# Kernel optimization log

Hardware: AMD Instinct MI355X
Metric: run time of the kernel (lower is better)

The kernel has to match this reference:

```python
import jax, jax.numpy as jnp
import numpy as np

N = 100      # num sensors/nodes
C = 32       # channels (hard-coded in module)
H = 512      # hidden_size (hard-coded)
T = 64       # window_size (lags)
B = 16       # batch
E = 2000     # edges = N * topk
HORIZON = 10


def _arma(x, ei, ew, W, V, b, n):
    # ARMAConv, num_stacks=1, num_layers=1, GELU act, dropout off (eval)
    h = x @ W                                    # (n, C)
    row, col = ei[0], ei[1]
    deg = jax.ops.segment_sum(ew, col, num_segments=n)
    dinv = jnp.where(deg > 0, 1.0 / jnp.sqrt(jnp.maximum(deg, 1e-12)), 0.0)
    norm = dinv[row] * ew * dinv[col]            # gcn_norm, no self loops
    agg = jax.ops.segment_sum(norm[:, None] * h[row], col, num_segments=n)
    return jax.nn.gelu(agg + x @ V + b, approximate=False)


def _lstm_step(h, c, xt, Wih, Whh, bih, bhh):
    g = xt @ Wih.T + h @ Whh.T + bih + bhh
    i, f, gg, o = jnp.split(g, 4, axis=-1)       # torch gate order i,f,g,o
    c = jax.nn.sigmoid(f) * c + jax.nn.sigmoid(i) * jnp.tanh(gg)
    h = jax.nn.sigmoid(o) * jnp.tanh(c)
    return h, c


def _lstm_layer(xs, Wih, Whh, bih, bhh):
    # xs: (T, B, in) -> outputs (T, B, H), final h
    Bn = xs.shape[1]
    init = (jnp.zeros((Bn, H), xs.dtype), jnp.zeros((Bn, H), xs.dtype))
    def step(carry, xt):
        hc = _lstm_step(carry[0], carry[1], xt, Wih, Whh, bih, bhh)
        return hc, hc[0]
    (hT, cT), hs = jax.lax.scan(step, init, xs)
    return hs, hT


def setup_inputs() -> dict:
    key = jax.random.key(0)
    ks = jax.random.split(key, 20)
    s = 0.05
    def nrm(k, shape):
        return jax.random.normal(k, shape, jnp.float32) * s
    ei = jax.random.randint(ks[1], (2, E), 0, N)
    ei = ei.at[0, 0].set(N - 1).at[1, 0].set(N - 1)  # ensure max node id present
    z = lambda *sh: jnp.zeros(sh, jnp.float32)
    return {
        "window": jax.random.normal(ks[0], (B * N, T), jnp.float32),
        "edge_index": ei,
        "edge_attr": jax.random.uniform(ks[2], (E,), jnp.float32),
        "W_embed": nrm(ks[3], (N, C)),
        "tg_w": nrm(ks[4], (1, C)), "tg_v": nrm(ks[5], (1, C)), "tg_b": z(C),
        "gnn_w": nrm(ks[6], (1, C)), "gnn_v": nrm(ks[7], (1, C)), "gnn_b": z(C),
        "lstm_Wih0": nrm(ks[8], (4 * H, N * C)), "lstm_Whh0": nrm(ks[9], (4 * H, H)),
        "lstm_bih0": z(4 * H), "lstm_bhh0": z(4 * H),
        "lstm_Wih1": nrm(ks[10], (4 * H, H)), "lstm_Whh1": nrm(ks[11], (4 * H, H)),
        "lstm_bih1": z(4 * H), "lstm_bhh1": z(4 * H),
        "c1_Wih": nrm(ks[12], (4 * H, N * C)), "c1_Whh": nrm(ks[13], (4 * H, H)),
        "c1_bih": z(4 * H), "c1_bhh": z(4 * H),
        "c2_Wih": nrm(ks[14], (4 * H, H)), "c2_Whh": nrm(ks[15], (4 * H, H)),
        "c2_bih": z(4 * H), "c2_bhh": z(4 * H),
        "Wp": nrm(ks[16], (N, H)), "bp": z(N),
    }


def _forward(edge_index, window, edge_attr, W_embed, tg_w, tg_v, tg_b,
             gnn_w, gnn_v, gnn_b,
             lstm_Wih0, lstm_Whh0, lstm_bih0, lstm_bhh0,
             lstm_Wih1, lstm_Whh1, lstm_bih1, lstm_bhh1,
             c1_Wih, c1_Whh, c1_bih, c1_bhh,
             c2_Wih, c2_Whh, c2_bih, c2_bhh, Wp, bp):
    BN = B * N
    # batch edges over B (offset b*N), exactly as the torch offset arithmetic
    bi = (edge_index[:, None, :] + (jnp.arange(B) * N)[None, :, None]).reshape(2, B * E)
    battr = jnp.tile(edge_attr, B)
    # temporal batching inside TGConv: offsets t*(B*N) on node-major flat x
    ti = (bi[:, None, :] + (jnp.arange(T) * BN)[None, :, None]).reshape(2, T * B * E)
    tattr = jnp.tile(battr, T)
    x = _arma(window.reshape(BN * T, 1), ti, tattr, tg_w, tg_v, tg_b, BN * T)  # (BN*T, C)
    x = x.reshape(B, N, T, C).transpose(0, 2, 1, 3) + W_embed                 # (B,T,N,C)
    x = x.reshape(B, T, N * C).transpose(1, 0, 2)                             # (T,B,NC)
    hs0, h1f = _lstm_layer(x, lstm_Wih0, lstm_Whh0, lstm_bih0, lstm_bhh0)
    hs1, h2f = _lstm_layer(hs0, lstm_Wih1, lstm_Whh1, lstm_bih1, lstm_bhh1)
    # original assigns (h_n, h_n): cell states seeded from hidden states
    def step(carry, _):
        h1, c1, h2, c2 = carry
        pred = h2 @ Wp.T + bp                      # (B, N)
        g = _arma(pred.reshape(BN, 1), bi, battr, gnn_w, gnn_v, gnn_b, BN)
        xin = (g.reshape(B, N, C) + W_embed).reshape(B, N * C)
        h1n, c1n = _lstm_step(h1, c1, xin, c1_Wih, c1_Whh, c1_bih, c1_bhh)
        h2n, c2n = _lstm_step(h2, c2, h1n, c2_Wih, c2_Whh, c2_bih, c2_bhh)
        return (h1n, c1n, h2n, c2n), pred.reshape(-1)
    _, preds = jax.lax.scan(step, (h1f, h1f, h2f, h2f), None, length=HORIZON)
    return preds.T                                  # (B*N, HORIZON)


def reference(window, edge_index, edge_attr, W_embed, tg_w, tg_v, tg_b,
              gnn_w, gnn_v, gnn_b,
              lstm_Wih0, lstm_Whh0, lstm_bih0, lstm_bhh0,
              lstm_Wih1, lstm_Whh1, lstm_bih1, lstm_bhh1,
              c1_Wih, c1_Whh, c1_bih, c1_bhh,
              c2_Wih, c2_Whh, c2_bih, c2_bhh, Wp, bp):
    return _forward(edge_index, window, edge_attr, W_embed, tg_w, tg_v, tg_b,
                    gnn_w, gnn_v, gnn_b,
                    lstm_Wih0, lstm_Whh0, lstm_bih0, lstm_bhh0,
                    lstm_Wih1, lstm_Whh1, lstm_bih1, lstm_bhh1,
                    c1_Wih, c1_Whh, c1_bih, c1_bhh,
                    c2_Wih, c2_Whh, c2_bih, c2_bhh, Wp, bp)
```

## Files before the change

### kernel.cpp

```cpp
#include <hip/hip_runtime.h>
#include <math.h>

#define TT 64
#define HZN 10
#define NBLK 256

__device__ __forceinline__ float sigm(float x) { return 1.f / (1.f + expf(-x)); }
__device__ __forceinline__ float gelu_f(float x) { return 0.5f * x * (1.f + erff(x * 0.70710678118654752f)); }

__device__ __forceinline__ float cLd(const float* p) {
  return __hip_atomic_load(p, __ATOMIC_RELAXED, __HIP_MEMORY_SCOPE_AGENT);
}
__device__ __forceinline__ void cSt(float* p, float v) {
  __hip_atomic_store(p, v, __ATOMIC_RELAXED, __HIP_MEMORY_SCOPE_AGENT);
}

__device__ __forceinline__ void gbar(unsigned* flags, unsigned* gen,
                                     int bid, int tid, unsigned& bgen) {
  ++bgen;
  __syncthreads();
  if (bid == 0) {
    if (tid > 0 && tid < NBLK) {
      while (__hip_atomic_load(&flags[tid], __ATOMIC_RELAXED, __HIP_MEMORY_SCOPE_AGENT) < bgen)
        __builtin_amdgcn_s_sleep(1);
    }
    __syncthreads();
    if (tid == 0)
      __hip_atomic_store(gen, bgen, __ATOMIC_RELAXED, __HIP_MEMORY_SCOPE_AGENT);
  } else {
    if (tid == 0) {
      asm volatile("s_waitcnt vmcnt(0)" ::: "memory");
      __hip_atomic_store(&flags[bid], bgen, __ATOMIC_RELAXED, __HIP_MEMORY_SCOPE_AGENT);
      while (__hip_atomic_load(gen, __ATOMIC_RELAXED, __HIP_MEMORY_SCOPE_AGENT) < bgen)
        __builtin_amdgcn_s_sleep(1);
    }
    __syncthreads();
  }
}

__device__ __forceinline__ void red32(float (&a)[4][4]) {
#pragma unroll
  for (int q = 0; q < 4; ++q)
#pragma unroll
    for (int r = 0; r < 4; ++r) {
      float v = a[q][r];
      v += __shfl_xor(v, 16); v += __shfl_xor(v, 8); v += __shfl_xor(v, 4);
      v += __shfl_xor(v, 2);  v += __shfl_xor(v, 1);
      a[q][r] = v;
    }
}

__device__ __forceinline__ void red64(float (&a)[4][4]) {
#pragma unroll
  for (int q = 0; q < 4; ++q)
#pragma unroll
    for (int r = 0; r < 4; ++r) {
      float v = a[q][r];
      v += __shfl_xor(v, 32); v += __shfl_xor(v, 16); v += __shfl_xor(v, 8);
      v += __shfl_xor(v, 4);  v += __shfl_xor(v, 2);  v += __shfl_xor(v, 1);
      a[q][r] = v;
    }
}

__global__ void setup_kernel(const int* __restrict__ ei, const float* __restrict__ ew,
                             int* __restrict__ cptr, int* __restrict__ csrc, float* __restrict__ cnorm) {
  __shared__ float deg[100];
  __shared__ float dinv[100];
  __shared__ int cnt[100];
  __shared__ int pos[100];
  __shared__ int ptr[101];
  const int t = threadIdx.x;
  if (t < 100) { deg[t] = 0.f; cnt[t] = 0; }
  __syncthreads();
  for (int e = t; e < 2000; e += 256) {
    int c = ei[2000 + e];
    atomicAdd(&deg[c], ew[e]);
    atomicAdd(&cnt[c], 1);
  }
  __syncthreads();
  if (t < 100) dinv[t] = (deg[t] > 0.f) ? 1.f / sqrtf(fmaxf(deg[t], 1e-12f)) : 0.f;
  if (t == 0) {
    ptr[0] = 0;
    for (int n = 0; n < 100; ++n) ptr[n + 1] = ptr[n] + cnt[n];
  }
  __syncthreads();
  if (t < 100) pos[t] = ptr[t];
  if (t < 101) cptr[t] = ptr[t];
  __syncthreads();
  for (int e = t; e < 2000; e += 256) {
    int r = ei[e], c = ei[2000 + e];
    int p = atomicAdd(&pos[c], 1);
    csrc[p] = r;
    cnorm[p] = dinv[r] * ew[e] * dinv[c];
  }
}

__global__ void xs_kernel(const float* __restrict__ win,
                          const int* __restrict__ cptr, const int* __restrict__ csrc,
                          const float* __restrict__ cnorm,
                          const float* __restrict__ tgw, const float* __restrict__ tgv,
                          const float* __restrict__ tgb, const float* __restrict__ Wemb,
                          float* __restrict__ XS) {
  const int g = blockIdx.x * 256 + threadIdx.x;
  if (g >= 102400) return;
  const int n2 = g % 100;
  const int base = g - n2;
  float s = 0.f;
  const int p0 = cptr[n2], p1 = cptr[n2 + 1];
  for (int p = p0; p < p1; ++p) s += cnorm[p] * win[base + csrc[p]];
  const float x = win[g];
  const int t = g % 64;
  const int bb = g / 6400;
  const int n = (g / 64) % 100;
  float* dst = XS + (size_t)(t * 16 + bb) * 3200 + n * 32;
  for (int c = 0; c < 32; ++c) {
    float v = s * tgw[c] + x * tgv[c] + tgb[c];
    dst[c] = gelu_f(v) + Wemb[n * 32 + c];
  }
}

__global__ __launch_bounds__(256) void g0_gemm(const float* __restrict__ XS, const float* __restrict__ W,
                                               const float* __restrict__ b1, const float* __restrict__ b2,
                                               float* __restrict__ G0) {
  __shared__ float As[16][68];
  __shared__ float Bs[16][68];
  const int tid = threadIdx.x;
  const int m0 = blockIdx.y * 64, n0 = blockIdx.x * 64;
  const int tx = tid & 15, ty = tid >> 4;
  const int lr = tid >> 2, lk = (tid & 3) * 4;
  float acc[4][4] = {};
  for (int k0 = 0; k0 < 3200; k0 += 16) {
    float4 av = *(const float4*)&XS[(size_t)(m0 + lr) * 3200 + k0 + lk];
    float4 bv = *(const float4*)&W[(size_t)(n0 + lr) * 3200 + k0 + lk];
    As[lk + 0][lr] = av.x; As[lk + 1][lr] = av.y; As[lk + 2][lr] = av.z; As[lk + 3][lr] = av.w;
    Bs[lk + 0][lr] = bv.x; Bs[lk + 1][lr] = bv.y; Bs[lk + 2][lr] = bv.z; Bs[lk + 3][lr] = bv.w;
    __syncthreads();
#pragma unroll
    for (int kk = 0; kk < 16; ++kk) {
      float4 a = *(const float4*)&As[kk][ty * 4];
      float4 b = *(const float4*)&Bs[kk][tx * 4];
      acc[0][0] += a.x * b.x; acc[0][1] += a.x * b.y; acc[0][2] += a.x * b.z; acc[0][3] += a.x * b.w;
      acc[1][0] += a.y * b.x; acc[1][1] += a.y * b.y; acc[1][2] += a.y * b.z; acc[1][3] += a.y * b.w;
      acc[2][0] += a.z * b.x; acc[2][1] += a.z * b.y; acc[2][2] += a.z * b.z; acc[2][3] += a.z * b.w;
      acc[3][0] += a.w * b.x; acc[3][1] += a.w * b.y; acc[3][2] += a.w * b.z; acc[3][3] += a.w * b.w;
    }
    __syncthreads();
  }
#pragma unroll
  for (int i = 0; i < 4; ++i) {
    const int m = m0 + ty * 4 + i;
#pragma unroll
    for (int j = 0; j < 4; ++j) {
      const int nn = n0 + tx * 4 + j;
      G0[(size_t)m * 2048 + nn] = acc[i][j] + b1[nn] + b2[nn];
    }
  }
}

struct CoopArgs {
  const float* G0;
  const float* Whh0;
  const float* Wih1; const float* Whh1; const float* bih1; const float* bhh1;
  const float* c1Wih; const float* c1Whh; const float* c1bih; const float* c1bhh;
  const float* c2Wih; const float* c2Whh; const float* c2bih; const float* c2bhh;
  const float* Wp; const float* bp;
  const float* gw; const float* gv; const float* gb;
  const float* Wemb;
  const int* cptr; const int* csrc; const float* cnorm;
  float* hs0; float* hL1; float* c0; float* cL1;
  float* h1d; float* c1b; float* h2d; float* c2b;
  float* pred; float* xin;
  unsigned* flags; unsigned* gen;
  float* out;
};

__global__ __launch_bounds__(512, 2) void coop_kernel(CoopArgs A) {
  __shared__ float lds[16384];
  const int tid = threadIdx.x;
  const int bid = blockIdx.x;
  const int gid = bid * 512 + tid;
  unsigned bgen = 0;

  const int layer = bid >> 7;
  const int ublk = bid & 127;
  const int u0 = ublk * 4;
  const int bg = tid >> 7;
  const int du = (tid >> 5) & 3;
  const int s = tid & 31;
  const int n_s = u0 + du;

  for (int t2 = 0; t2 <= TT; ++t2) {
    if (layer == 0) {
      if (t2 < TT) {
        const int t0 = t2;
        float acc[4][4] = {};
        if (t0 > 0) {
          const float* src = A.hs0 + (size_t)(t0 - 1) * 8192;
          for (int i = tid; i < 8192; i += 512) lds[i] = cLd(&src[i]);
        }
        __syncthreads();
        if (t0 > 0) {
          for (int jj = 0; jj < 16; ++jj) {
            const int j = jj * 32 + s;
            const float w0 = A.Whh0[(n_s) * 512 + j];
            const float w1 = A.Whh0[(512 + n_s) * 512 + j];
            const float w2 = A.Whh0[(1024 + n_s) * 512 + j];
            const float w3 = A.Whh0[(1536 + n_s) * 512 + j];
#pragma unroll
            for (int br = 0; br < 4; ++br) {
              const float hv = lds[(bg * 4 + br) * 512 + j];
              acc[0][br] += w0 * hv; acc[1][br] += w1 * hv;
              acc[2][br] += w2 * hv; acc[3][br] += w3 * hv;
            }
          }
        }
        red32(acc);
        if (s == 0) {
#pragma unroll
          for (int br = 0; br < 4; ++br) {
            const int b = bg * 4 + br;
            const float* g0r = A.G0 + (size_t)(t0 * 16 + b) * 2048;
            const float gi = acc[0][br] + g0r[n_s];
            const float gf = acc[1][br] + g0r[512 + n_s];
            const float gg = acc[2][br] + g0r[1024 + n_s];
            const float go = acc[3][br] + g0r[1536 + n_s];
            const float cp = (t0 > 0) ? A.c0[b * 512 + n_s] : 0.f;
            const float cn = sigm(gf) * cp + sigm(gi) * tanhf(gg);
            const float hn = sigm(go) * tanhf(cn);
            A.c0[b * 512 + n_s] = cn;
            cSt(&A.hs0[(size_t)t0 * 8192 + b * 512 + n_s], hn);
          }
        }
      }
    } else {
      if (t2 >= 1) {
        const int t1 = t2 - 1;
        float acc[4][4] = {};
        {
          const float* sA = A.hs0 + (size_t)t1 * 8192;
          for (int i = tid; i < 8192; i += 512) lds[i] = cLd(&sA[i]);
          if (t1 > 0) {
            const float* sB = A.hL1 + (t1 & 1) * 8192;
            for (int i = tid; i < 8192; i += 512) lds[8192 + i] = cLd(&sB[i]);
          }
        }
        __syncthreads();
        for (int jj = 0; jj < 16; ++jj) {
          const int j = jj * 32 + s;
          const float wa0 = A.Wih1[(n_s) * 512 + j];
          const float wa1 = A.Wih1[(512 + n_s) * 512 + j];
          const float wa2 = A.Wih1[(1024 + n_s) * 512 + j];
          const float wa3 = A.Wih1[(1536 + n_s) * 512 + j];
#pragma unroll
          for (int br = 0; br < 4; ++br) {
            const float ha = lds[(bg * 4 + br) * 512 + j];
            acc[0][br] += wa0 * ha; acc[1][br] += wa1 * ha;
            acc[2][br] += wa2 * ha; acc[3][br] += wa3 * ha;
          }
          if (t1 > 0) {
            const float wb0 = A.Whh1[(n_s) * 512 + j];
            const float wb1 = A.Whh1[(512 + n_s) * 512 + j];
            const float wb2 = A.Whh1[(1024 + n_s) * 512 + j];
            const float wb3 = A.Whh1[(1536 + n_s) * 512 + j];
#pragma unroll
            for (int br = 0; br < 4; ++br) {
              const float hb = lds[8192 + (bg * 4 + br) * 512 + j];
              acc[0][br] += wb0 * hb; acc[1][br] += wb1 * hb;
              acc[2][br] += wb2 * hb; acc[3][br] += wb3 * hb;
            }
          }
        }
        red32(acc);
        if (s == 0) {
#pragma unroll
          for (int br = 0; br < 4; ++br) {
            const int b = bg * 4 + br;
            const float gi = acc[0][br] + A.bih1[n_s] + A.bhh1[n_s];
            const float gf = acc[1][br] + A.bih1[512 + n_s] + A.bhh1[512 + n_s];
            const float gg = acc[2][br] + A.bih1[1024 + n_s] + A.bhh1[1024 + n_s];
            const float go = acc[3][br] + A.bih1[1536 + n_s] + A.bhh1[1536 + n_s];
            const float cp = (t1 > 0) ? A.cL1[b * 512 + n_s] : 0.f;
            const float cn = sigm(gf) * cp + sigm(gi) * tanhf(gg);
            const float hn = sigm(go) * tanhf(cn);
            A.cL1[b * 512 + n_s] = cn;
            cSt(&A.hL1[((t1 & 1) ^ 1) * 8192 + b * 512 + n_s], hn);
          }
        }
      }
    }
    gbar(A.flags, A.gen, bid, tid, bgen);
  }

  if (gid < 8192) {
    const float h1v = cLd(&A.hs0[(size_t)63 * 8192 + gid]);
    cSt(&A.h1d[gid], h1v); cSt(&A.c1b[gid], h1v);
    const float h2v = cLd(&A.hL1[gid]);
    cSt(&A.h2d[gid], h2v); cSt(&A.c2b[gid], h2v);
  }
  gbar(A.flags, A.gen, bid, tid, bgen);

  for (int hz = 0; hz < HZN; ++hz) {
    const int cur = hz & 1, nxt = cur ^ 1;

    if (gid < 25600) {
      const int bn = gid >> 4, sp = gid & 15;
      const int b = bn / 100, n = bn % 100;
      const float* h2 = A.h2d + cur * 8192 + b * 512;
      const float* wp = A.Wp + n * 512;
      float a = 0.f;
      for (int jj = 0; jj < 32; ++jj) { const int j = jj * 16 + sp; a += cLd(&h2[j]) * wp[j]; }
      a += __shfl_xor(a, 1); a += __shfl_xor(a, 2); a += __shfl_xor(a, 4); a += __shfl_xor(a, 8);
      if (sp == 0) {
        const float v = a + A.bp[n];
        cSt(&A.pred[bn], v);
        A.out[bn * HZN + hz] = v;
      }
    }
    gbar(A.flags, A.gen, bid, tid, bgen);

    if (bid < 100) {
      for (int i = tid; i < 1600; i += 512) lds[i] = cLd(&A.pred[i]);
      __syncthreads();
      const int g2 = bid * 512 + tid;
      const int b = g2 / 3200, rem = g2 % 3200;
      const int n = rem >> 5, c = rem & 31;
      float s2 = 0.f;
      const int p0 = A.cptr[n], p1 = A.cptr[n + 1];
      for (int p = p0; p < p1; ++p) s2 += A.cnorm[p] * lds[b * 100 + A.csrc[p]];
      const float pv = lds[b * 100 + n];
      const float v = s2 * A.gw[c] + pv * A.gv[c] + A.gb[c];
      cSt(&A.xin[g2], gelu_f(v) + A.Wemb[n * 32 + c]);
    }
    gbar(A.flags, A.gen, bid, tid, bgen);

    {
      const int uc = bid & 63, bq = bid >> 6;
      const int u = tid >> 6, sl = tid & 63;
      const int n = uc * 8 + u;
      float* xinl = lds;
      float* h1l = lds + 12800;
      for (int i = tid; i < 12800; i += 512) xinl[i] = cLd(&A.xin[(size_t)bq * 12800 + i]);
      for (int i = tid; i < 2048; i += 512) h1l[i] = cLd(&A.h1d[cur * 8192 + bq * 2048 + i]);
      __syncthreads();
      float acc[4][4] = {};
      for (int jj = 0; jj < 50; ++jj) {
        const int j = jj * 64 + sl;
        const float w0 = A.c1Wih[(size_t)(n) * 3200 + j];
        const float w1 = A.c1Wih[(size_t)(512 + n) * 3200 + j];
        const float w2 = A.c1Wih[(size_t)(1024 + n) * 3200 + j];
        const float w3 = A.c1Wih[(size_t)(1536 + n) * 3200 + j];
#pragma unroll
        for (int bl = 0; bl < 4; ++bl) {
          const float xv = xinl[bl * 3200 + j];
          acc[0][bl] += w0 * xv; acc[1][bl] += w1 * xv;
          acc[2][bl] += w2 * xv; acc[3][bl] += w3 * xv;
        }
      }
      for (int jj = 0; jj < 8; ++jj) {
        const int j = jj * 64 + sl;
        const float w0 = A.c1Whh[(n) * 512 + j];
        const float w1 = A.c1Whh[(512 + n) * 512 + j];
        const float w2 = A.c1Whh[(1024 + n) * 512 + j];
        const float w3 = A.c1Whh[(1536 + n) * 512 + j];
#pragma unroll
        for (int bl = 0; bl < 4; ++bl) {
          const float hv = h1l[bl * 512 + j];
          acc[0][bl] += w0 * hv; acc[1][bl] += w1 * hv;
          acc[2][bl] += w2 * hv; acc[3][bl] += w3 * hv;
        }
      }
      red64(acc);
      if (sl == 0) {
#pragma unroll
        for (int bl = 0; bl < 4; ++bl) {
          const int b = bq * 4 + bl;
          const float gi = acc[0][bl] + A.c1bih[n] + A.c1bhh[n];
          const float gf = acc[1][bl] + A.c1bih[512 + n] + A.c1bhh[512 + n];
          const float gg = acc[2][bl] + A.c1bih[1024 + n] + A.c1bhh[1024 + n];
          const float go = acc[3][bl] + A.c1bih[1536 + n] + A.c1bhh[1536 + n];
          const float cp = cLd(&A.c1b[b * 512 + n]);
          const float cn = sigm(gf) * cp + sigm(gi) * tanhf(gg);
          const float hn = sigm(go) * tanhf(cn);
          cSt(&A.c1b[b * 512 + n], cn);
          cSt(&A.h1d[nxt * 8192 + b * 512 + n], hn);
        }
      }
    }
    gbar(A.flags, A.gen, bid, tid, bgen);

    {
      const int uc = bid & 63, bq = bid >> 6;
      const int u = tid >> 6, sl = tid & 63;
      const int n = uc * 8 + u;
      float* hAl = lds;
      float* hBl = lds + 2048;
      for (int i = tid; i < 2048; i += 512) {
        hAl[i] = cLd(&A.h1d[nxt * 8192 + bq * 2048 + i]);
        hBl[i] = cLd(&A.h2d[cur * 8192 + bq * 2048 + i]);
      }
      __syncthreads();
      float acc[4][4] = {};
      for (int jj = 0; jj < 8; ++jj) {
        const int j = jj * 64 + sl;
        const float wa0 = A.c2Wih[(n) * 512 + j];
        const float wa1 = A.c2Wih[(512 + n) * 512 + j];
        const float wa2 = A.c2Wih[(1024 + n) * 512 + j];
        const float wa3 = A.c2Wih[(1536 + n) * 512 + j];
        const float wb0 = A.c2Whh[(n) * 512 + j];
        const float wb1 = A.c2Whh[(512 + n) * 512 + j];
        const float wb2 = A.c2Whh[(1024 + n) * 512 + j];
        const float wb3 = A.c2Whh[(1536 + n) * 512 + j];
#pragma unroll
        for (int bl = 0; bl < 4; ++bl) {
          const float ha = hAl[bl * 512 + j];
          const float hb = hBl[bl * 512 + j];
          acc[0][bl] += wa0 * ha + wb0 * hb;
          acc[1][bl] += wa1 * ha + wb1 * hb;
          acc[2][bl] += wa2 * ha + wb2 * hb;
          acc[3][bl] += wa3 * ha + wb3 * hb;
        }
      }
      red64(acc);
      if (sl == 0) {
#pragma unroll
        for (int bl = 0; bl < 4; ++bl) {
          const int b = bq * 4 + bl;
          const float gi = acc[0][bl] + A.c2bih[n] + A.c2bhh[n];
          const float gf = acc[1][bl] + A.c2bih[512 + n] + A.c2bhh[512 + n];
          const float gg = acc[2][bl] + A.c2bih[1024 + n] + A.c2bhh[1024 + n];
          const float go = acc[3][bl] + A.c2bih[1536 + n] + A.c2bhh[1536 + n];
          const float cp = cLd(&A.c2b[b * 512 + n]);
          const float cn = sigm(gf) * cp + sigm(gi) * tanhf(gg);
          const float hn = sigm(go) * tanhf(cn);
          cSt(&A.c2b[b * 512 + n], cn);
          cSt(&A.h2d[nxt * 8192 + b * 512 + n], hn);
        }
      }
    }
    gbar(A.flags, A.gen, bid, tid, bgen);
  }
}

extern "C" void kernel_launch(void* const* d_in, const int* in_sizes, int n_in,
                              void* d_out, int out_size, void* d_ws, size_t ws_size,
                              hipStream_t stream) {
  (void)in_sizes; (void)n_in; (void)out_size; (void)ws_size;
  const float* window = (const float*)d_in[0];
  const int* ei = (const int*)d_in[1];
  const float* ew = (const float*)d_in[2];
  const float* Wemb = (const float*)d_in[3];
  const float* tgw = (const float*)d_in[4];
  const float* tgv = (const float*)d_in[5];
  const float* tgb = (const float*)d_in[6];
  const float* gw = (const float*)d_in[7];
  const float* gv = (const float*)d_in[8];
  const float* gb = (const float*)d_in[9];
  const float* Wih0 = (const float*)d_in[10];
  const float* Whh0 = (const float*)d_in[11];
  const float* bih0 = (const float*)d_in[12];
  const float* bhh0 = (const float*)d_in[13];
  const float* Wih1 = (const float*)d_in[14];
  const float* Whh1 = (const float*)d_in[15];
  const float* bih1 = (const float*)d_in[16];
  const float* bhh1 = (const float*)d_in[17];
  const float* c1Wih = (const float*)d_in[18];
  const float* c1Whh = (const float*)d_in[19];
  const float* c1bih = (const float*)d_in[20];
  const float* c1bhh = (const float*)d_in[21];
  const float* c2Wih = (const float*)d_in[22];
  const float* c2Whh = (const float*)d_in[23];
  const float* c2bih = (const float*)d_in[24];
  const float* c2bhh = (const float*)d_in[25];
  const float* Wp = (const float*)d_in[26];
  const float* bp = (const float*)d_in[27];

  char* w = (char*)d_ws;
  size_t off = 0;
  auto alloc = [&](size_t bytes) { void* p = w + off; off = (off + bytes + 255) & ~(size_t)255; return p; };
  int* cptr = (int*)alloc(101 * 4);
  int* csrc = (int*)alloc(2000 * 4);
  float* cnorm = (float*)alloc(2000 * 4);
  float* XS = (float*)alloc((size_t)1024 * 3200 * 4);
  float* G0 = (float*)alloc((size_t)1024 * 2048 * 4);
  float* hs0 = (float*)alloc((size_t)64 * 8192 * 4);
  float* hL1 = (float*)alloc((size_t)2 * 8192 * 4);
  float* c0 = (float*)alloc((size_t)8192 * 4);
  float* cL1 = (float*)alloc((size_t)8192 * 4);
  float* h1d = (float*)alloc((size_t)2 * 8192 * 4);
  float* c1b = (float*)alloc((size_t)8192 * 4);
  float* h2d = (float*)alloc((size_t)2 * 8192 * 4);
  float* c2b = (float*)alloc((size_t)8192 * 4);
  float* pred = (float*)alloc(1600 * 4);
  float* xin = (float*)alloc((size_t)51200 * 4);
  unsigned* flags = (unsigned*)alloc(NBLK * 4);
  unsigned* gen = (unsigned*)alloc(64);

  hipMemsetAsync(flags, 0, NBLK * 4, stream);
  hipMemsetAsync(gen, 0, 4, stream);

  setup_kernel<<<1, 256, 0, stream>>>(ei, ew, cptr, csrc, cnorm);
  xs_kernel<<<400, 256, 0, stream>>>(window, cptr, csrc, cnorm, tgw, tgv, tgb, Wemb, XS);
  g0_gemm<<<dim3(32, 16), 256, 0, stream>>>(XS, Wih0, bih0, bhh0, G0);

  CoopArgs A;
  A.G0 = G0; A.Whh0 = Whh0;
  A.Wih1 = Wih1; A.Whh1 = Whh1; A.bih1 = bih1; A.bhh1 = bhh1;
  A.c1Wih = c1Wih; A.c1Whh = c1Whh; A.c1bih = c1bih; A.c1bhh = c1bhh;
  A.c2Wih = c2Wih; A.c2Whh = c2Whh; A.c2bih = c2bih; A.c2bhh = c2bhh;
  A.Wp = Wp; A.bp = bp; A.gw = gw; A.gv = gv; A.gb = gb; A.Wemb = Wemb;
  A.cptr = cptr; A.csrc = csrc; A.cnorm = cnorm;
  A.hs0 = hs0; A.hL1 = hL1; A.c0 = c0; A.cL1 = cL1;
  A.h1d = h1d; A.c1b = c1b; A.h2d = h2d; A.c2b = c2b;
  A.pred = pred; A.xin = xin;
  A.flags = flags; A.gen = gen;
  A.out = (float*)d_out;
  void* params[] = { &A };
  hipLaunchCooperativeKernel(coop_kernel, dim3(NBLK), dim3(512), params, 0, stream);
}
```

Baseline: 1.900 ms.

## Rewrite recurrent coop kernel with bf16-packed weights and per-batch flag sync

Recurrent weights are pre-packed to bf16 pairs by new pack kernels, which halves weight bandwidth in the recurrent loops. The encoder phase now assigns blocks per (batch, unit-slice) and synchronises through per-batch producer/consumer flags instead of a grid-wide barrier each timestep. This lets the two layers pipeline against each other. The decoder phase is restructured with LDS staging and a new thread-to-unit mapping, and some hidden states are exchanged in bf16. This risks accuracy loss from bf16 weights and adds pack-kernel launches on every call.

After: 2.621 ms. 1.38x slower.

```diff
diff --git a/kernel.cpp b/kernel.cpp
--- a/kernel.cpp
+++ b/kernel.cpp
@@ -1,7 +1,6 @@
 #include <hip/hip_runtime.h>
 #include <math.h>
 
-#define TT 64
 #define HZN 10
 #define NBLK 256
 
@@ -14,52 +13,43 @@
 __device__ __forceinline__ void cSt(float* p, float v) {
   __hip_atomic_store(p, v, __ATOMIC_RELAXED, __HIP_MEMORY_SCOPE_AGENT);
 }
-
-__device__ __forceinline__ void gbar(unsigned* flags, unsigned* gen,
-                                     int bid, int tid, unsigned& bgen) {
+__device__ __forceinline__ unsigned cLdU(const unsigned* p) {
+  return __hip_atomic_load(p, __ATOMIC_RELAXED, __HIP_MEMORY_SCOPE_AGENT);
+}
+__device__ __forceinline__ void cStU(unsigned* p, unsigned v) {
+  __hip_atomic_store(p, v, __ATOMIC_RELAXED, __HIP_MEMORY_SCOPE_AGENT);
+}
+__device__ __forceinline__ void vfence() {
+  asm volatile("s_waitcnt vmcnt(0)" ::: "memory");
+}
+
+__device__ __forceinline__ float blo(unsigned u) { return __uint_as_float(u << 16); }
+__device__ __forceinline__ float bhi(unsigned u) { return __uint_as_float(u & 0xffff0000u); }
+__device__ __forceinline__ unsigned bfu(float x) {
+  unsigned u = __float_as_uint(x);
+  return (u + 0x7fffu + ((u >> 16) & 1u)) >> 16;
+}
+__device__ __forceinline__ unsigned packbf(float a, float b) {
+  return bfu(a) | (bfu(b) << 16);
+}
+
+__device__ __forceinline__ void gbar(unsigned* flags, unsigned* gen, int bid, int tid, unsigned& bgen) {
   ++bgen;
+  vfence();
   __syncthreads();
   if (bid == 0) {
     if (tid > 0 && tid < NBLK) {
-      while (__hip_atomic_load(&flags[tid], __ATOMIC_RELAXED, __HIP_MEMORY_SCOPE_AGENT) < bgen)
-        __builtin_amdgcn_s_sleep(1);
+      while (cLdU(&flags[tid]) < bgen) __builtin_amdgcn_s_sleep(1);
     }
     __syncthreads();
-    if (tid == 0)
-      __hip_atomic_store(gen, bgen, __ATOMIC_RELAXED, __HIP_MEMORY_SCOPE_AGENT);
+    if (tid == 0) cStU(gen, bgen);
   } else {
     if (tid == 0) {
-      asm volatile("s_waitcnt vmcnt(0)" ::: "memory");
-      __hip_atomic_store(&flags[bid], bgen, __ATOMIC_RELAXED, __HIP_MEMORY_SCOPE_AGENT);
-      while (__hip_atomic_load(gen, __ATOMIC_RELAXED, __HIP_MEMORY_SCOPE_AGENT) < bgen)
-        __builtin_amdgcn_s_sleep(1);
+      cStU(&flags[bid], bgen);
+      while (cLdU(gen) < bgen) __builtin_amdgcn_s_sleep(1);
     }
     __syncthreads();
   }
-}
-
-__device__ __forceinline__ void red32(float (&a)[4][4]) {
-#pragma unroll
-  for (int q = 0; q < 4; ++q)
-#pragma unroll
-    for (int r = 0; r < 4; ++r) {
-      float v = a[q][r];
-      v += __shfl_xor(v, 16); v += __shfl_xor(v, 8); v += __shfl_xor(v, 4);
-      v += __shfl_xor(v, 2);  v += __shfl_xor(v, 1);
-      a[q][r] = v;
-    }
-}
-
-__device__ __forceinline__ void red64(float (&a)[4][4]) {
-#pragma unroll
-  for (int q = 0; q < 4; ++q)
-#pragma unroll
-    for (int r = 0; r < 4; ++r) {
-      float v = a[q][r];
-      v += __shfl_xor(v, 32); v += __shfl_xor(v, 16); v += __shfl_xor(v, 8);
-      v += __shfl_xor(v, 4);  v += __shfl_xor(v, 2);  v += __shfl_xor(v, 1);
-      a[q][r] = v;
-    }
 }
 
 __global__ void setup_kernel(const int* __restrict__ ei, const float* __restrict__ ew,
@@ -93,6 +83,18 @@
     csrc[p] = r;
     cnorm[p] = dinv[r] * ew[e] * dinv[c];
   }
+}
+
+__global__ void pack_rows(const float* __restrict__ A, const float* __restrict__ B,
+                          int Ka, int Kb, int rows, unsigned* __restrict__ out) {
+  int K2 = (Ka + Kb) >> 1;
+  long idx = (long)blockIdx.x * 256 + threadIdx.x;
+  if (idx >= (long)rows * K2) return;
+  int row = idx / K2, q = idx - (long)row * K2;
+  int j0 = 2 * q;
+  float a = (j0 < Ka) ? A[(long)row * Ka + j0] : B[(long)row * Kb + (j0 - Ka)];
+  float b = (j0 + 1 < Ka) ? A[(long)row * Ka + j0 + 1] : B[(long)row * Kb + (j0 + 1 - Ka)];
+  out[idx] = packbf(a, b);
 }
 
 __global__ void xs_kernel(const float* __restrict__ win,
@@ -159,285 +161,340 @@
 
 struct CoopArgs {
   const float* G0;
-  const float* Whh0;
-  const float* Wih1; const float* Whh1; const float* bih1; const float* bhh1;
-  const float* c1Wih; const float* c1Whh; const float* c1bih; const float* c1bhh;
-  const float* c2Wih; const float* c2Whh; const float* c2bih; const float* c2bhh;
+  const unsigned* W0p;
+  const unsigned* W1p;
+  const float* bih1; const float* bhh1;
+  const unsigned* c1Wih2;
+  const unsigned* c1Whh2;
+  const float* c1bih; const float* c1bhh;
+  const unsigned* c2W2;
+  const float* c2bih; const float* c2bhh;
   const float* Wp; const float* bp;
   const float* gw; const float* gv; const float* gb;
   const float* Wemb;
   const int* cptr; const int* csrc; const float* cnorm;
-  float* hs0; float* hL1; float* c0; float* cL1;
-  float* h1d; float* c1b; float* h2d; float* c2b;
-  float* pred; float* xin;
-  unsigned* flags; unsigned* gen;
+  float* hs0;
+  float* h1ex;
+  unsigned* h1pk;
+  unsigned* h2pk;
+  float* h2f;
+  unsigned* F0;
+  unsigned* F1;
+  unsigned* bflags; unsigned* gen;
   float* out;
 };
 
-__global__ __launch_bounds__(512, 2) void coop_kernel(CoopArgs A) {
-  __shared__ float lds[16384];
+__global__ __launch_bounds__(512, 1) void coop_kernel(CoopArgs A) {
+  extern __shared__ float lds[];
   const int tid = threadIdx.x;
   const int bid = blockIdx.x;
-  const int gid = bid * 512 + tid;
   unsigned bgen = 0;
 
-  const int layer = bid >> 7;
-  const int ublk = bid & 127;
-  const int u0 = ublk * 4;
-  const int bg = tid >> 7;
-  const int du = (tid >> 5) & 3;
-  const int s = tid & 31;
-  const int n_s = u0 + du;
-
-  for (int t2 = 0; t2 <= TT; ++t2) {
-    if (layer == 0) {
-      if (t2 < TT) {
-        const int t0 = t2;
-        float acc[4][4] = {};
-        if (t0 > 0) {
-          const float* src = A.hs0 + (size_t)(t0 - 1) * 8192;
-          for (int i = tid; i < 8192; i += 512) lds[i] = cLd(&src[i]);
+  if (bid < 128) {
+    const int b = bid >> 3, j = bid & 7;
+    const int r = tid >> 1, hf = tid & 1;
+    const uint4* wp = (const uint4*)A.W0p + ((size_t)((r >> 6) * 512 + j * 64 + (r & 63))) * 64 + hf * 32;
+    float* hl = lds;
+    float* gl = lds + 512;
+    float c0r = 0.f;
+    for (int t = 0; t < 64; ++t) {
+      if (t > 0) {
+        if (tid < 8) {
+          while (cLdU(&A.F0[b * 8 + tid]) < (unsigned)t) __builtin_amdgcn_s_sleep(1);
         }
         __syncthreads();
-        if (t0 > 0) {
-          for (int jj = 0; jj < 16; ++jj) {
-            const int j = jj * 32 + s;
-            const float w0 = A.Whh0[(n_s) * 512 + j];
-            const float w1 = A.Whh0[(512 + n_s) * 512 + j];
-            const float w2 = A.Whh0[(1024 + n_s) * 512 + j];
-            const float w3 = A.Whh0[(1536 + n_s) * 512 + j];
-#pragma unroll
-            for (int br = 0; br < 4; ++br) {
-              const float hv = lds[(bg * 4 + br) * 512 + j];
-              acc[0][br] += w0 * hv; acc[1][br] += w1 * hv;
-              acc[2][br] += w2 * hv; acc[3][br] += w3 * hv;
+        hl[tid] = cLd(&A.hs0[((size_t)(t - 1) * 16 + b) * 512 + tid]);
+        __syncthreads();
+      }
+      float acc = 0.f;
+      if (t > 0) {
+        const float2* h2 = (const float2*)hl + hf * 128;
+#pragma unroll 8
+        for (int i = 0; i < 32; ++i) {
+          uint4 w = wp[i];
+          float2 ha = h2[4 * i], hb = h2[4 * i + 1], hc = h2[4 * i + 2], hd = h2[4 * i + 3];
+          acc += blo(w.x) * ha.x + bhi(w.x) * ha.y;
+          acc += blo(w.y) * hb.x + bhi(w.y) * hb.y;
+          acc += blo(w.z) * hc.x + bhi(w.z) * hc.y;
+          acc += blo(w.w) * hd.x + bhi(w.w) * hd.y;
+        }
+      }
+      acc += __shfl_xor(acc, 1);
+      if (hf == 0) gl[r] = acc;
+      __syncthreads();
+      if (tid < 64) {
+        const float* g0r = A.G0 + ((size_t)t * 16 + b) * 2048 + j * 64;
+        float gi = gl[tid] + g0r[tid];
+        float gf = gl[64 + tid] + g0r[512 + tid];
+        float gg = gl[128 + tid] + g0r[1024 + tid];
+        float go = gl[192 + tid] + g0r[1536 + tid];
+        c0r = sigm(gf) * c0r + sigm(gi) * tanhf(gg);
+        float hn = sigm(go) * tanhf(c0r);
+        cSt(&A.hs0[((size_t)t * 16 + b) * 512 + j * 64 + tid], hn);
+      }
+      vfence();
+      __syncthreads();
+      if (tid == 0) cStU(&A.F0[b * 8 + j], t + 1);
+    }
+  } else {
+    const int b = (bid - 128) >> 3, j = bid & 7;
+    const int r = tid >> 1, hf = tid & 1;
+    const int wrow = (r >> 6) * 512 + j * 64 + (r & 63);
+    const uint4* wp = (const uint4*)A.W1p + (size_t)wrow * 128 + hf * 64;
+    float* hl = lds;
+    float* gl = lds + 1024;
+    float c1s = 0.f;
+    for (int t = 0; t < 64; ++t) {
+      if (tid < 8) {
+        while (cLdU(&A.F0[b * 8 + tid]) < (unsigned)(t + 1)) __builtin_amdgcn_s_sleep(1);
+        if (t > 0) {
+          while (cLdU(&A.F1[b * 8 + tid]) < (unsigned)t) __builtin_amdgcn_s_sleep(1);
+        }
+      }
+      __syncthreads();
+      hl[tid] = cLd(&A.hs0[((size_t)t * 16 + b) * 512 + tid]);
+      hl[512 + tid] = (t > 0) ? cLd(&A.h1ex[(((t - 1) & 1) * 16 + b) * 512 + tid]) : 0.f;
+      __syncthreads();
+      float acc = 0.f;
+      {
+        const float2* h2 = (const float2*)hl + hf * 256;
+#pragma unroll 8
+        for (int i = 0; i < 64; ++i) {
+          uint4 w = wp[i];
+          float2 ha = h2[4 * i], hb = h2[4 * i + 1], hc = h2[4 * i + 2], hd = h2[4 * i + 3];
+          acc += blo(w.x) * ha.x + bhi(w.x) * ha.y;
+          acc += blo(w.y) * hb.x + bhi(w.y) * hb.y;
+          acc += blo(w.z) * hc.x + bhi(w.z) * hc.y;
+          acc += blo(w.w) * hd.x + bhi(w.w) * hd.y;
+        }
+      }
+      acc += __shfl_xor(acc, 1);
+      if (hf == 0) gl[r] = acc;
+      __syncthreads();
+      if (tid < 64) {
+        int uu = j * 64 + tid;
+        float gi = gl[tid] + A.bih1[uu] + A.bhh1[uu];
+        float gf = gl[64 + tid] + A.bih1[512 + uu] + A.bhh1[512 + uu];
+        float gg = gl[128 + tid] + A.bih1[1024 + uu] + A.bhh1[1024 + uu];
+        float go = gl[192 + tid] + A.bih1[1536 + uu] + A.bhh1[1536 + uu];
+        c1s = sigm(gf) * c1s + sigm(gi) * tanhf(gg);
+        float hn = sigm(go) * tanhf(c1s);
+        cSt(&A.h1ex[((t & 1) * 16 + b) * 512 + uu], hn);
+      }
+      vfence();
+      __syncthreads();
+      if (tid == 0) cStU(&A.F1[b * 8 + j], t + 1);
+    }
+  }
+
+  gbar(A.bflags, A.gen, bid, tid, bgen);
+
+  const int u0 = bid * 2;
+  float* xinl = lds;
+  float* h1l = lds + 25600;
+  float* predl = lds + 29696;
+  float* s2l = lds + 30496;
+  float* gatel = lds + 31296;
+
+  float c1reg[2];
+  float c2reg = 0.f;
+  if (tid < 16) {
+#pragma unroll
+    for (int p = 0; p < 2; ++p) {
+      int bl = tid >> 1, du = tid & 1;
+      c1reg[p] = cLd(&A.hs0[((size_t)63 * 16 + p * 8 + bl) * 512 + u0 + du]);
+    }
+  }
+  if (tid < 32) {
+    int bl = tid >> 1, du = tid & 1;
+    c2reg = cLd(&A.h1ex[(1 * 16 + bl) * 512 + u0 + du]);
+  }
+
+  for (int hz = 0; hz < HZN; ++hz) {
+    const int cur = hz & 1, nxt = cur ^ 1;
+
+#pragma unroll
+    for (int p = 0; p < 2; ++p) {
+      const int B0 = p * 8;
+      for (int k = 0; k < 8; ++k) {
+        int i = k * 512 + tid;
+        int bb = i >> 9, u = i & 511;
+        float v = (hz == 0) ? cLd(&A.h1ex[(1 * 16 + B0 + bb) * 512 + u])
+                            : cLd(&A.h2f[((size_t)cur * 16 + B0 + bb) * 512 + u]);
+        xinl[i] = v;
+      }
+      for (int k = 0; k < 4; ++k) {
+        int i = k * 512 + tid;
+        int bb = i >> 8, pp = i & 255;
+        float x0, x1;
+        if (hz == 0) {
+          x0 = cLd(&A.hs0[((size_t)63 * 16 + B0 + bb) * 512 + 2 * pp]);
+          x1 = cLd(&A.hs0[((size_t)63 * 16 + B0 + bb) * 512 + 2 * pp + 1]);
+        } else {
+          unsigned pk = cLdU(&A.h1pk[((size_t)cur * 16 + B0 + bb) * 256 + pp]);
+          x0 = blo(pk); x1 = bhi(pk);
+        }
+        h1l[bb * 512 + 2 * pp] = x0;
+        h1l[bb * 512 + 2 * pp + 1] = x1;
+      }
+      __syncthreads();
+      {
+        const int g16 = tid >> 4, ln = tid & 15;
+        for (int it = 0; it < 4; ++it) {
+          const int n2 = it * 32 + g16;
+          if (n2 < 100) {
+            float w[32];
+#pragma unroll
+            for (int kk = 0; kk < 32; ++kk) w[kk] = A.Wp[n2 * 512 + kk * 16 + ln];
+            for (int bb = 0; bb < 8; ++bb) {
+              float a = 0.f;
+#pragma unroll
+              for (int kk = 0; kk < 32; ++kk) a += w[kk] * xinl[bb * 512 + kk * 16 + ln];
+              a += __shfl_xor(a, 1); a += __shfl_xor(a, 2);
+              a += __shfl_xor(a, 4); a += __shfl_xor(a, 8);
+              if (ln == 0) predl[bb * 100 + n2] = a + A.bp[n2];
             }
           }
         }
-        red32(acc);
-        if (s == 0) {
-#pragma unroll
-          for (int br = 0; br < 4; ++br) {
-            const int b = bg * 4 + br;
-            const float* g0r = A.G0 + (size_t)(t0 * 16 + b) * 2048;
-            const float gi = acc[0][br] + g0r[n_s];
-            const float gf = acc[1][br] + g0r[512 + n_s];
-            const float gg = acc[2][br] + g0r[1024 + n_s];
-            const float go = acc[3][br] + g0r[1536 + n_s];
-            const float cp = (t0 > 0) ? A.c0[b * 512 + n_s] : 0.f;
-            const float cn = sigm(gf) * cp + sigm(gi) * tanhf(gg);
-            const float hn = sigm(go) * tanhf(cn);
-            A.c0[b * 512 + n_s] = cn;
-            cSt(&A.hs0[(size_t)t0 * 8192 + b * 512 + n_s], hn);
+      }
+      __syncthreads();
+      if (bid == 0) {
+        for (int i = tid; i < 800; i += 512) {
+          int bb = i / 100, n2 = i - bb * 100;
+          A.out[((B0 + bb) * 100 + n2) * HZN + hz] = predl[i];
+        }
+      }
+      for (int i = tid; i < 800; i += 512) {
+        int bb = i / 100, n2 = i - bb * 100;
+        float s2 = 0.f;
+        for (int pp = A.cptr[n2]; pp < A.cptr[n2 + 1]; ++pp)
+          s2 += A.cnorm[pp] * predl[bb * 100 + A.csrc[pp]];
+        s2l[i] = s2;
+      }
+      __syncthreads();
+      for (int k = 0; k < 50; ++k) {
+        int i2 = k * 512 + tid;
+        int bb = i2 / 3200, rem = i2 - bb * 3200;
+        int n2 = rem >> 5, cc = rem & 31;
+        float v = s2l[bb * 100 + n2] * A.gw[cc] + predl[bb * 100 + n2] * A.gv[cc] + A.gb[cc];
+        xinl[i2] = gelu_f(v) + A.Wemb[n2 * 32 + cc];
+      }
+      __syncthreads();
+      {
+        float acc[8] = {};
+        const int r_ = tid >> 6, ks = tid & 63;
+        const int wrow = (r_ >> 1) * 512 + u0 + (r_ & 1);
+        for (int jj = 0; jj < 25; ++jj) {
+          int pi = jj * 64 + ks;
+          unsigned w = A.c1Wih2[(size_t)wrow * 1600 + pi];
+          float wl = blo(w), wh = bhi(w);
+#pragma unroll
+          for (int bb = 0; bb < 8; ++bb) {
+            float2 x = *(float2*)&xinl[bb * 3200 + 2 * pi];
+            acc[bb] += wl * x.x + wh * x.y;
           }
         }
-      }
-    } else {
-      if (t2 >= 1) {
-        const int t1 = t2 - 1;
-        float acc[4][4] = {};
-        {
-          const float* sA = A.hs0 + (size_t)t1 * 8192;
-          for (int i = tid; i < 8192; i += 512) lds[i] = cLd(&sA[i]);
-          if (t1 > 0) {
-            const float* sB = A.hL1 + (t1 & 1) * 8192;
-            for (int i = tid; i < 8192; i += 512) lds[8192 + i] = cLd(&sB[i]);
+        for (int jj = 0; jj < 4; ++jj) {
+          int pi = jj * 64 + ks;
+          unsigned w = A.c1Whh2[wrow * 256 + pi];
+          float wl = blo(w), wh = bhi(w);
+#pragma unroll
+          for (int bb = 0; bb < 8; ++bb) {
+            float2 x = *(float2*)&h1l[bb * 512 + 2 * pi];
+            acc[bb] += wl * x.x + wh * x.y;
           }
         }
-        __syncthreads();
-        for (int jj = 0; jj < 16; ++jj) {
-          const int j = jj * 32 + s;
-          const float wa0 = A.Wih1[(n_s) * 512 + j];
-          const float wa1 = A.Wih1[(512 + n_s) * 512 + j];
-          const float wa2 = A.Wih1[(1024 + n_s) * 512 + j];
-          const float wa3 = A.Wih1[(1536 + n_s) * 512 + j];
-#pragma unroll
-          for (int br = 0; br < 4; ++br) {
-            const float ha = lds[(bg * 4 + br) * 512 + j];
-            acc[0][br] += wa0 * ha; acc[1][br] += wa1 * ha;
-            acc[2][br] += wa2 * ha; acc[3][br] += wa3 * ha;
-          }
-          if (t1 > 0) {
-            const float wb0 = A.Whh1[(n_s) * 512 + j];
-            const float wb1 = A.Whh1[(512 + n_s) * 512 + j];
-            const float wb2 = A.Whh1[(1024 + n_s) * 512 + j];
-            const float wb3 = A.Whh1[(1536 + n_s) * 512 + j];
-#pragma unroll
-            for (int br = 0; br < 4; ++br) {
-              const float hb = lds[8192 + (bg * 4 + br) * 512 + j];
-              acc[0][br] += wb0 * hb; acc[1][br] += wb1 * hb;
-              acc[2][br] += wb2 * hb; acc[3][br] += wb3 * hb;
-            }
-          }
-        }
-        red32(acc);
-        if (s == 0) {
-#pragma unroll
-          for (int br = 0; br < 4; ++br) {
-            const int b = bg * 4 + br;
-            const float gi = acc[0][br] + A.bih1[n_s] + A.bhh1[n_s];
-            const float gf = acc[1][br] + A.bih1[512 + n_s] + A.bhh1[512 + n_s];
-            const float gg = acc[2][br] + A.bih1[1024 + n_s] + A.bhh1[1024 + n_s];
-            const float go = acc[3][br] + A.bih1[1536 + n_s] + A.bhh1[1536 + n_s];
-            const float cp = (t1 > 0) ? A.cL1[b * 512 + n_s] : 0.f;
-            const float cn = sigm(gf) * cp + sigm(gi) * tanhf(gg);
-            const float hn = sigm(go) * tanhf(cn);
-            A.cL1[b * 512 + n_s] = cn;
-            cSt(&A.hL1[((t1 & 1) ^ 1) * 8192 + b * 512 + n_s], hn);
-          }
-        }
-      }
-    }
-    gbar(A.flags, A.gen, bid, tid, bgen);
-  }
-
-  if (gid < 8192) {
-    const float h1v = cLd(&A.hs0[(size_t)63 * 8192 + gid]);
-    cSt(&A.h1d[gid], h1v); cSt(&A.c1b[gid], h1v);
-    const float h2v = cLd(&A.hL1[gid]);
-    cSt(&A.h2d[gid], h2v); cSt(&A.c2b[gid], h2v);
-  }
-  gbar(A.flags, A.gen, bid, tid, bgen);
-
-  for (int hz = 0; hz < HZN; ++hz) {
-    const int cur = hz & 1, nxt = cur ^ 1;
-
-    if (gid < 25600) {
-      const int bn = gid >> 4, sp = gid & 15;
-      const int b = bn / 100, n = bn % 100;
-      const float* h2 = A.h2d + cur * 8192 + b * 512;
-      const float* wp = A.Wp + n * 512;
-      float a = 0.f;
-      for (int jj = 0; jj < 32; ++jj) { const int j = jj * 16 + sp; a += cLd(&h2[j]) * wp[j]; }
-      a += __shfl_xor(a, 1); a += __shfl_xor(a, 2); a += __shfl_xor(a, 4); a += __shfl_xor(a, 8);
-      if (sp == 0) {
-        const float v = a + A.bp[n];
-        cSt(&A.pred[bn], v);
-        A.out[bn * HZN + hz] = v;
-      }
-    }
-    gbar(A.flags, A.gen, bid, tid, bgen);
-
-    if (bid < 100) {
-      for (int i = tid; i < 1600; i += 512) lds[i] = cLd(&A.pred[i]);
-      __syncthreads();
-      const int g2 = bid * 512 + tid;
-      const int b = g2 / 3200, rem = g2 % 3200;
-      const int n = rem >> 5, c = rem & 31;
-      float s2 = 0.f;
-      const int p0 = A.cptr[n], p1 = A.cptr[n + 1];
-      for (int p = p0; p < p1; ++p) s2 += A.cnorm[p] * lds[b * 100 + A.csrc[p]];
-      const float pv = lds[b * 100 + n];
-      const float v = s2 * A.gw[c] + pv * A.gv[c] + A.gb[c];
-      cSt(&A.xin[g2], gelu_f(v) + A.Wemb[n * 32 + c]);
-    }
-    gbar(A.flags, A.gen, bid, tid, bgen);
+#pragma unroll
+        for (int bb = 0; bb < 8; ++bb) {
+          float v = acc[bb];
+          v += __shfl_xor(v, 32); v += __shfl_xor(v, 16); v += __shfl_xor(v, 8);
+          v += __shfl_xor(v, 4); v += __shfl_xor(v, 2); v += __shfl_xor(v, 1);
+          acc[bb] = v;
+        }
+        if (ks == 0) {
+#pragma unroll
+          for (int bb = 0; bb < 8; ++bb) gatel[r_ * 8 + bb] = acc[bb];
+        }
+      }
+      __syncthreads();
+      if (tid < 16) {
+        int bl = tid >> 1, du = tid & 1;
+        int uu = u0 + du;
+        float gi = gatel[(0 + du) * 8 + bl] + A.c1bih[uu] + A.c1bhh[uu];
+        float gf = gatel[(2 + du) * 8 + bl] + A.c1bih[512 + uu] + A.c1bhh[512 + uu];
+        float gg = gatel[(4 + du) * 8 + bl] + A.c1bih[1024 + uu] + A.c1bhh[1024 + uu];
+        float go = gatel[(6 + du) * 8 + bl] + A.c1bih[1536 + uu] + A.c1bhh[1536 + uu];
+        float cn = sigm(gf) * c1reg[p] + sigm(gi) * tanhf(gg);
+        float hn = sigm(go) * tanhf(cn);
+        c1reg[p] = cn;
+        float ho = __shfl(hn, tid ^ 1);
+        if (du == 0) cStU(&A.h1pk[((size_t)nxt * 16 + B0 + bl) * 256 + bid], packbf(hn, ho));
+      }
+      __syncthreads();
+    }
+    gbar(A.bflags, A.gen, bid, tid, bgen);
 
     {
-      const int uc = bid & 63, bq = bid >> 6;
-      const int u = tid >> 6, sl = tid & 63;
-      const int n = uc * 8 + u;
-      float* xinl = lds;
-      float* h1l = lds + 12800;
-      for (int i = tid; i < 12800; i += 512) xinl[i] = cLd(&A.xin[(size_t)bq * 12800 + i]);
-      for (int i = tid; i < 2048; i += 512) h1l[i] = cLd(&A.h1d[cur * 8192 + bq * 2048 + i]);
-      __syncthreads();
-      float acc[4][4] = {};
-      for (int jj = 0; jj < 50; ++jj) {
-        const int j = jj * 64 + sl;
-        const float w0 = A.c1Wih[(size_t)(n) * 3200 + j];
-        const float w1 = A.c1Wih[(size_t)(512 + n) * 3200 + j];
-        const float w2 = A.c1Wih[(size_t)(1024 + n) * 3200 + j];
-        const float w3 = A.c1Wih[(size_t)(1536 + n) * 3200 + j];
-#pragma unroll
-        for (int bl = 0; bl < 4; ++bl) {
-          const float xv = xinl[bl * 3200 + j];
-          acc[0][bl] += w0 * xv; acc[1][bl] += w1 * xv;
-          acc[2][bl] += w2 * xv; acc[3][bl] += w3 * xv;
-        }
-      }
+      unsigned* h1b = (unsigned*)lds;
+      unsigned* h2b = (unsigned*)lds + 4096;
+      for (int k = 0; k < 8; ++k) {
+        int i = k * 512 + tid;
+        int bb = i >> 8, pp = i & 255;
+        h1b[i] = cLdU(&A.h1pk[((size_t)nxt * 16 + bb) * 256 + pp]);
+        unsigned v2;
+        if (hz == 0) {
+          float x0 = cLd(&A.h1ex[(16 + bb) * 512 + 2 * pp]);
+          float x1 = cLd(&A.h1ex[(16 + bb) * 512 + 2 * pp + 1]);
+          v2 = packbf(x0, x1);
+        } else {
+          v2 = cLdU(&A.h2pk[((size_t)cur * 16 + bb) * 256 + pp]);
+        }
+        h2b[i] = v2;
+      }
+      __syncthreads();
+      float acc[16] = {};
+      const int r_ = tid >> 6, ks = tid & 63;
+      const int wrow = (r_ >> 1) * 512 + u0 + (r_ & 1);
       for (int jj = 0; jj < 8; ++jj) {
-        const int j = jj * 64 + sl;
-        const float w0 = A.c1Whh[(n) * 512 + j];
-        const float w1 = A.c1Whh[(512 + n) * 512 + j];
-        const float w2 = A.c1Whh[(1024 + n) * 512 + j];
-        const float w3 = A.c1Whh[(1536 + n) * 512 + j];
-#pragma unroll
-        for (int bl = 0; bl < 4; ++bl) {
-          const float hv = h1l[bl * 512 + j];
-          acc[0][bl] += w0 * hv; acc[1][bl] += w1 * hv;
-          acc[2][bl] += w2 * hv; acc[3][bl] += w3 * hv;
-        }
-      }
-      red64(acc);
-      if (sl == 0) {
-#pragma unroll
-        for (int bl = 0; bl < 4; ++bl) {
-          const int b = bq * 4 + bl;
-          const float gi = acc[0][bl] + A.c1bih[n] + A.c1bhh[n];
-          const float gf = acc[1][bl] + A.c1bih[512 + n] + A.c1bhh[512 + n];
-          const float gg = acc[2][bl] + A.c1bih[1024 + n] + A.c1bhh[1024 + n];
-          const float go = acc[3][bl] + A.c1bih[1536 + n] + A.c1bhh[1536 + n];
-          const float cp = cLd(&A.c1b[b * 512 + n]);
-          const float cn = sigm(gf) * cp + sigm(gi) * tanhf(gg);
-          const float hn = sigm(go) * tanhf(cn);
-          cSt(&A.c1b[b * 512 + n], cn);
-          cSt(&A.h1d[nxt * 8192 + b * 512 + n], hn);
-        }
-      }
-    }
-    gbar(A.flags, A.gen, bid, tid, bgen);
-
-    {
-      const int uc = bid & 63, bq = bid >> 6;
-      const int u = tid >> 6, sl = tid & 63;
-      const int n = uc * 8 + u;
-      float* hAl = lds;
-      float* hBl = lds + 2048;
-      for (int i = tid; i < 2048; i += 512) {
-        hAl[i] = cLd(&A.h1d[nxt * 8192 + bq * 2048 + i]);
-        hBl[i] = cLd(&A.h2d[cur * 8192 + bq * 2048 + i]);
-      }
-      __syncthreads();
-      float acc[4][4] = {};
-      for (int jj = 0; jj < 8; ++jj) {
-        const int j = jj * 64 + sl;
-        const float wa0 = A.c2Wih[(n) * 512 + j];
-        const float wa1 = A.c2Wih[(512 + n) * 512 + j];
-        const float wa2 = A.c2Wih[(1024 + n) * 512 + j];
-        const float wa3 = A.c2Wih[(1536 + n) * 512 + j];
-        const float wb0 = A.c2Whh[(n) * 512 + j];
-        const float wb1 = A.c2Whh[(512 + n) * 512 + j];
-        const float wb2 = A.c2Whh[(1024 + n) * 512 + j];
-        const float wb3 = A.c2Whh[(1536 + n) * 512 + j];
-#pragma unroll
-        for (int bl = 0; bl < 4; ++bl) {
-          const float ha = hAl[bl * 512 + j];
-          const float hb = hBl[bl * 512 + j];
-          acc[0][bl] += wa0 * ha + wb0 * hb;
-          acc[1][bl] += wa1 * ha + wb1 * hb;
-          acc[2][bl] += wa2 * ha + wb2 * hb;
-          acc[3][bl] += wa3 * ha + wb3 * hb;
-        }
-      }
-      red64(acc);
-      if (sl == 0) {
-#pragma unroll
-        for (int bl = 0; bl < 4; ++bl) {
-          const int b = bq * 4 + bl;
-          const float gi = acc[0][bl] + A.c2bih[n] + A.c2bhh[n];
-          const float gf = acc[1][bl] + A.c2bih[512 + n] + A.c2bhh[512 + n];
-          const float gg = acc[2][bl] + A.c2bih[1024 + n] + A.c2bhh[1024 + n];
-          const float go = acc[3][bl] + A.c2bih[1536 + n] + A.c2bhh[1536 + n];
-          const float cp = cLd(&A.c2b[b * 512 + n]);
-          const float cn = sigm(gf) * cp + sigm(gi) * tanhf(gg);
-          const float hn = sigm(go) * tanhf(cn);
-          cSt(&A.c2b[b * 512 + n], cn);
-          cSt(&A.h2d[nxt * 8192 + b * 512 + n], hn);
-        }
-      }
-    }
-    gbar(A.flags, A.gen, bid, tid, bgen);
+        int pi = jj * 64 + ks;
+        unsigned w = A.c2W2[wrow * 512 + pi];
+        float wl = blo(w), wh = bhi(w);
+        const unsigned* hsrc = (pi < 256) ? h1b : (h2b - 256);
+#pragma unroll
+        for (int bb = 0; bb < 16; ++bb) {
+          unsigned hv = hsrc[bb * 256 + pi];
+          acc[bb] += wl * blo(hv) + wh * bhi(hv);
+        }
+      }
+#pragma unroll
+      for (int bb = 0; bb < 16; ++bb) {
+        float v = acc[bb];
+        v += __shfl_xor(v, 32); v += __shfl_xor(v, 16); v += __shfl_xor(v, 8);
+        v += __shfl_xor(v, 4); v += __shfl_xor(v, 2); v += __shfl_xor(v, 1);
+        acc[bb] = v;
+      }
+      if (ks == 0) {
+#pragma unroll
+        for (int bb = 0; bb < 16; ++bb) gatel[r_ * 16 + bb] = acc[bb];
+      }
+      __syncthreads();
+      if (tid < 32) {
+        int bl = tid >> 1, du = tid & 1;
+        int uu = u0 + du;
+        float gi = gatel[(0 + du) * 16 + bl] + A.c2bih[uu] + A.c2bhh[uu];
+        float gf = gatel[(2 + du) * 16 + bl] + A.c2bih[512 + uu] + A.c2bhh[512 + uu];
+        float gg = gatel[(4 + du) * 16 + bl] + A.c2bih[1024 + uu] + A.c2bhh[1024 + uu];
+        float go = gatel[(6 + du) * 16 + bl] + A.c2bih[1536 + uu] + A.c2bhh[1536 + uu];
+        float cn = sigm(gf) * c2reg + sigm(gi) * tanhf(gg);
+        float hn = sigm(go) * tanhf(cn);
+        c2reg = cn;
+        cSt(&A.h2f[((size_t)nxt * 16 + bl) * 512 + uu], hn);
+        float ho = __shfl(hn, tid ^ 1);
+        if (du == 0) cStU(&A.h2pk[((size_t)nxt * 16 + bl) * 256 + bid], packbf(hn, ho));
+      }
+      __syncthreads();
+    }
+    gbar(A.bflags, A.gen, bid, tid, bgen);
   }
 }
 
@@ -482,38 +539,43 @@
   float* cnorm = (float*)alloc(2000 * 4);
   float* XS = (float*)alloc((size_t)1024 * 3200 * 4);
   float* G0 = (float*)alloc((size_t)1024 * 2048 * 4);
-  float* hs0 = (float*)alloc((size_t)64 * 8192 * 4);
-  float* hL1 = (float*)alloc((size_t)2 * 8192 * 4);
-  float* c0 = (float*)alloc((size_t)8192 * 4);
-  float* cL1 = (float*)alloc((size_t)8192 * 4);
-  float* h1d = (float*)alloc((size_t)2 * 8192 * 4);
-  float* c1b = (float*)alloc((size_t)8192 * 4);
-  float* h2d = (float*)alloc((size_t)2 * 8192 * 4);
-  float* c2b = (float*)alloc((size_t)8192 * 4);
-  float* pred = (float*)alloc(1600 * 4);
-  float* xin = (float*)alloc((size_t)51200 * 4);
-  unsigned* flags = (unsigned*)alloc(NBLK * 4);
-  unsigned* gen = (unsigned*)alloc(64);
-
-  hipMemsetAsync(flags, 0, NBLK * 4, stream);
-  hipMemsetAsync(gen, 0, 4, stream);
+  unsigned* W0p = (unsigned*)alloc((size_t)2048 * 256 * 4);
+  unsigned* W1p = (unsigned*)alloc((size_t)2048 * 512 * 4);
+  unsigned* c1Wih2 = (unsigned*)alloc((size_t)2048 * 1600 * 4);
+  unsigned* c1Whh2 = (unsigned*)alloc((size_t)2048 * 256 * 4);
+  unsigned* c2W2 = (unsigned*)alloc((size_t)2048 * 512 * 4);
+  float* hs0 = (float*)alloc((size_t)64 * 16 * 512 * 4);
+  float* h1ex = (float*)alloc((size_t)2 * 16 * 512 * 4);
+  unsigned* h1pk = (unsigned*)alloc((size_t)2 * 16 * 256 * 4);
+  unsigned* h2pk = (unsigned*)alloc((size_t)2 * 16 * 256 * 4);
+  float* h2f = (float*)alloc((size_t)2 * 16 * 512 * 4);
+  unsigned* flagzone = (unsigned*)alloc((128 + 128 + 256 + 16) * 4);
+  unsigned* F0 = flagzone;
+  unsigned* F1 = flagzone + 128;
+  unsigned* bflags = flagzone + 256;
+  unsigned* gen = flagzone + 512;
+
+  hipMemsetAsync(flagzone, 0, (128 + 128 + 256 + 16) * 4, stream);
 
   setup_kernel<<<1, 256, 0, stream>>>(ei, ew, cptr, csrc, cnorm);
+  pack_rows<<<(2048 * 256 + 255) / 256, 256, 0, stream>>>(Whh0, nullptr, 512, 0, 2048, W0p);
+  pack_rows<<<(2048 * 512 + 255) / 256, 256, 0, stream>>>(Wih1, Whh1, 512, 512, 2048, W1p);
+  pack_rows<<<(int)(((size_t)2048 * 1600 + 255) / 256), 256, 0, stream>>>(c1Wih, nullptr, 3200, 0, 2048, c1Wih2);
+  pack_rows<<<(2048 * 256 + 255) / 256, 256, 0, stream>>>(c1Whh, nullptr, 512, 0, 2048, c1Whh2);
+  pack_rows<<<(2048 * 512 + 255) / 256, 256, 0, stream>>>(c2Wih, c2Whh, 512, 512, 2048, c2W2);
   xs_kernel<<<400, 256, 0, stream>>>(window, cptr, csrc, cnorm, tgw, tgv, tgb, Wemb, XS);
   g0_gemm<<<dim3(32, 16), 256, 0, stream>>>(XS, Wih0, bih0, bhh0, G0);
 
   CoopArgs A;
-  A.G0 = G0; A.Whh0 = Whh0;
-  A.Wih1 = Wih1; A.Whh1 = Whh1; A.bih1 = bih1; A.bhh1 = bhh1;
-  A.c1Wih = c1Wih; A.c1Whh = c1Whh; A.c1bih = c1bih; A.c1bhh = c1bhh;
-  A.c2Wih = c2Wih; A.c2Whh = c2Whh; A.c2bih = c2bih; A.c2bhh = c2bhh;
+  A.G0 = G0; A.W0p = W0p; A.W1p = W1p;
+  A.bih1 = bih1; A.bhh1 = bhh1;
+  A.c1Wih2 = c1Wih2; A.c1Whh2 = c1Whh2; A.c1bih = c1bih; A.c1bhh = c1bhh;
+  A.c2W2 = c2W2; A.c2bih = c2bih; A.c2bhh = c2bhh;
   A.Wp = Wp; A.bp = bp; A.gw = gw; A.gv = gv; A.gb = gb; A.Wemb = Wemb;
   A.cptr = cptr; A.csrc = csrc; A.cnorm = cnorm;
-  A.hs0 = hs0; A.hL1 = hL1; A.c0 = c0; A.cL1 = cL1;
-  A.h1d = h1d; A.c1b = c1b; A.h2d = h2d; A.c2b = c2b;
-  A.pred = pred; A.xin = xin;
-  A.flags = flags; A.gen = gen;
+  A.hs0 = hs0; A.h1ex = h1ex; A.h1pk = h1pk; A.h2pk = h2pk; A.h2f = h2f;
+  A.F0 = F0; A.F1 = F1; A.bflags = bflags; A.gen = gen;
   A.out = (float*)d_out;
   void* params[] = { &A };
-  hipLaunchCooperativeKernel(coop_kernel, dim3(NBLK), dim3(512), params, 0, stream);
-}
+  hipLaunchCooperativeKernel(coop_kernel, dim3(NBLK), dim3(512), params, 31424 * 4, stream);
+}
```
